# Kernel optimization log

Hardware: AMD Instinct MI355X
Metric: run time of the kernel (lower is better)

The kernel has to match this reference:

```python
import jax, jax.numpy as jnp
import numpy as np

EPS = 1e-5


def setup_inputs() -> dict:
    key = jax.random.key(0)
    ks = jax.random.split(key, 6)
    B, H, W, C = 4, 64, 64, 64
    x_in = jax.random.normal(ks[0], (B, H, W, C), dtype=jnp.float32)
    scale = 1.0 / np.sqrt(C)
    w1 = jax.random.normal(ks[1], (C, C), dtype=jnp.float32) * scale
    w2 = jax.random.normal(ks[2], (C, C), dtype=jnp.float32) * scale
    w3 = jax.random.normal(ks[3], (C, C), dtype=jnp.float32) * scale
    w4 = jax.random.normal(ks[4], (C, C), dtype=jnp.float32) * scale
    zeros = jnp.zeros((C,), dtype=jnp.float32)
    return {
        "x_in": x_in,
        "w1": w1, "w2": w2, "w3": w3, "w4": w4,
        "b1": zeros, "b2": zeros, "b3": zeros, "b4": zeros,
        "gamma": jnp.ones((C,), dtype=jnp.float32),
        "beta": zeros,
    }


def reference(x_in, w1, w2, w3, w4, b1, b2, b3, b4, gamma, beta):
    B, H, W, C = x_in.shape
    # BatchNorm over batch + spatial dims, per channel (training-mode batch stats)
    mean = jnp.mean(x_in, axis=(0, 1, 2))            # [C]
    var = jnp.var(x_in, axis=(0, 1, 2))              # [C]
    x = (x_in - mean) * jax.lax.rsqrt(var + EPS) * gamma + beta
    # QKV projections
    q = jnp.einsum('bhwc,cC->bhwC', x, w1) + b1
    k = jnp.einsum('bhwc,cC->bhwC', x, w2) + b2
    v = jnp.einsum('bhwc,cC->bhwC', x, w3) + b3
    # Full spatial attention: [B, H, W, H, W]
    sdpa = jnp.einsum('bhwc,bHWc->bhwHW', q, k) / jnp.sqrt(jnp.float32(C))
    sdpa = jax.nn.softmax(sdpa.reshape(B, H, W, H * W), axis=-1)
    sdpa = sdpa.reshape(B, H, W, H, W)
    x = jnp.einsum('bhwHW,bHWc->bhwc', sdpa, v)
    # Output projection + residual
    x = jnp.einsum('bhwc,cC->bhwC', x, w4) + b4
    return x + x_in
```

## Files before the change

### kernel.cpp

```cpp
#include <hip/hip_runtime.h>

typedef _Float16 f16;
typedef _Float16 half8 __attribute__((ext_vector_type(8)));
typedef float f32x4 __attribute__((ext_vector_type(4)));
typedef float f32x16 __attribute__((ext_vector_type(16)));
typedef unsigned u32x4 __attribute__((ext_vector_type(4)));

#define LDW 72

__global__ __launch_bounds__(256) void k_bnstats(const float* __restrict__ x, float* __restrict__ part){
    __shared__ float red[512];
    int t = threadIdx.x;
    int c = t & 63, rg = t >> 6;
    int rb = blockIdx.x * 64;
    float s = 0.f, s2 = 0.f;
    for(int r = rg; r < 64; r += 4){
        float v = x[(rb + r) * 64 + c];
        s += v; s2 += v * v;
    }
    red[t] = s; red[256 + t] = s2;
    __syncthreads();
    if(t < 128){
        int c2 = t & 63, h = t >> 6;
        float a = red[h * 256 + c2] + red[h * 256 + c2 + 64] + red[h * 256 + c2 + 128] + red[h * 256 + c2 + 192];
        part[blockIdx.x * 128 + t] = a;
    }
}

__global__ __launch_bounds__(256) void k_qkv(
    const float* __restrict__ x,
    const float* __restrict__ w1, const float* __restrict__ w2, const float* __restrict__ w3,
    const float* __restrict__ b1, const float* __restrict__ b2, const float* __restrict__ b3,
    const float* __restrict__ gamma, const float* __restrict__ beta,
    const float* __restrict__ part,
    f16* __restrict__ Q, f16* __restrict__ Kx, f16* __restrict__ Vt){
    __shared__ f16 wT[3 * 64 * LDW];
    __shared__ float sc[64], sh[64], bb[3][64];
    __shared__ float psum[128];
    int t = threadIdx.x;
    for(int i = t; i < 3 * 4096; i += 256){
        int j = i >> 12, e = i & 4095, k = e >> 6, n = e & 63;
        const float* wp = (j == 0) ? w1 : ((j == 1) ? w2 : w3);
        wT[j * 64 * LDW + n * LDW + k] = (f16)wp[e];
    }
    if(t < 128){
        float a0 = 0.f, a1 = 0.f, a2 = 0.f, a3 = 0.f;
        for(int b = 0; b < 256; b += 4){
            a0 += part[b * 128 + t];       a1 += part[(b + 1) * 128 + t];
            a2 += part[(b + 2) * 128 + t]; a3 += part[(b + 3) * 128 + t];
        }
        psum[t] = (a0 + a1) + (a2 + a3);
    }
    __syncthreads();
    if(t < 64){
        float mean = psum[t] * (1.f / 16384.f);
        float var  = psum[64 + t] * (1.f / 16384.f) - mean * mean;
        float s = gamma[t] * rsqrtf(var + 1e-5f);
        sc[t] = s;
        sh[t] = beta[t] - mean * s;
        bb[0][t] = b1[t]; bb[1][t] = b2[t]; bb[2][t] = b3[t];
    }
    __syncthreads();
    int w = t >> 6, lane = t & 63, quad = lane >> 4, l15 = lane & 15;
    int rowb = blockIdx.x * 64 + w * 16;
    int arow = rowb + l15;
    half8 a[2];
    #pragma unroll
    for(int kc = 0; kc < 2; kc++){
        f32x4 x0 = *(const f32x4*)&x[arow * 64 + kc * 32 + quad * 8];
        f32x4 x1 = *(const f32x4*)&x[arow * 64 + kc * 32 + quad * 8 + 4];
        half8 h;
        #pragma unroll
        for(int j = 0; j < 8; j++){
            int c = kc * 32 + quad * 8 + j;
            float xv = (j < 4) ? x0[j & 3] : x1[j & 3];
            h[j] = (f16)(xv * sc[c] + sh[c]);
        }
        a[kc] = h;
    }
    const f32x4 vzero = {0.f, 0.f, 0.f, 0.f};
    f32x4 acc[3][4];
    #pragma unroll
    for(int m = 0; m < 3; m++){
        #pragma unroll
        for(int nt = 0; nt < 4; nt++){
            acc[m][nt] = vzero;
            #pragma unroll
            for(int kc = 0; kc < 2; kc++){
                half8 bfr = *(half8*)&wT[m * 64 * LDW + (nt * 16 + l15) * LDW + kc * 32 + quad * 8];
                acc[m][nt] = __builtin_amdgcn_mfma_f32_16x16x32_f16(a[kc], bfr, acc[m][nt], 0, 0, 0);
            }
        }
    }
    const float qs = 0.18033688011112043f;
    #pragma unroll
    for(int nt = 0; nt < 4; nt++){
        #pragma unroll
        for(int r = 0; r < 4; r++){
            int row = rowb + quad * 4 + r;
            int col = nt * 16 + l15;
            Q[row * 64 + col]  = (f16)((acc[0][nt][r] + bb[0][col]) * qs);
            Kx[row * 64 + col] = (f16)(acc[1][nt][r] + bb[1][col]);
            Vt[((row >> 12) * 64 + col) * 4096 + (row & 4095)] = (f16)(acc[2][nt][r] + bb[2][col]);
        }
    }
}

__global__ __launch_bounds__(256, 4) void k_attn(
    const f16* __restrict__ Q, const f16* __restrict__ Kx, const f16* __restrict__ Vt,
    f16* __restrict__ Oph, float* __restrict__ lw){
    __shared__ f16 KV[2][2 * 64 * LDW];
    __shared__ float lred[4][32];
    int t = threadIdx.x;
    int kq = blockIdx.x & 7, qg = blockIdx.x >> 3;
    int b = qg >> 5;
    int w = t >> 6, lane = t & 63, l31 = lane & 31, hi = lane >> 5;
    int qrow0 = qg * 128 + w * 32;
    const int BUF = 2 * 64 * LDW;

    half8 aq[4];
    #pragma unroll
    for(int dc = 0; dc < 4; dc++)
        aq[dc] = *(const half8*)&Q[(qrow0 + l31) * 64 + dc * 16 + hi * 8];

    const f16* gsrc[4];
    int loff[4], gstep[4];
    #pragma unroll
    for(int i = 0; i < 4; i++){
        int idx = t + i * 256;
        int rr = (idx >> 3) & 63, c8 = idx & 7, kt0 = kq * 8;
        if(idx < 512){
            loff[i] = rr * LDW + c8 * 8;
            gsrc[i] = &Kx[(b * 4096 + kt0 * 64 + rr) * 64 + c8 * 8];
            gstep[i] = 64 * 64;
        } else {
            loff[i] = 64 * LDW + rr * LDW + c8 * 8;
            gsrc[i] = &Vt[(b * 64 + rr) * 4096 + kt0 * 64 + c8 * 8];
            gstep[i] = 64;
        }
    }
    half8 pre[4];
    #pragma unroll
    for(int i = 0; i < 4; i++){ pre[i] = *(const half8*)gsrc[i]; gsrc[i] += gstep[i]; }
    #pragma unroll
    for(int i = 0; i < 4; i++) *(half8*)&KV[0][loff[i]] = pre[i];

    f32x16 o[2];
    #pragma unroll
    for(int dt = 0; dt < 2; dt++)
        #pragma unroll
        for(int r = 0; r < 16; r++) o[dt][r] = 0.f;
    float lp = 0.f;

    __syncthreads();
    int cur = 0;
    for(int j = 0; j < 8; j++){
        if(j < 7){
            #pragma unroll
            for(int i = 0; i < 4; i++){ pre[i] = *(const half8*)gsrc[i]; gsrc[i] += gstep[i]; }
        }
        const f16* Kb = &KV[0][0] + cur * BUF;
        const f16* Vb = Kb + 64 * LDW;
        #pragma unroll
        for(int kt = 0; kt < 2; kt++){
            half8 ak[4];
            #pragma unroll
            for(int dc = 0; dc < 4; dc++)
                ak[dc] = *(const half8*)&Kb[(kt * 32 + l31) * LDW + dc * 16 + hi * 8];
            half8 vb[2][2];
            #pragma unroll
            for(int kc = 0; kc < 2; kc++)
                #pragma unroll
                for(int dt = 0; dt < 2; dt++)
                    vb[kc][dt] = *(const half8*)&Vb[(dt * 32 + l31) * LDW + kt * 32 + kc * 16 + hi * 8];
            f32x16 s;
            #pragma unroll
            for(int r = 0; r < 16; r++) s[r] = 0.f;
            #pragma unroll
            for(int dc = 0; dc < 4; dc++)
                s = __builtin_amdgcn_mfma_f32_32x32x16_f16(ak[dc], aq[dc], s, 0, 0, 0);
            float pf[16], ls = 0.f;
            #pragma unroll
            for(int r = 0; r < 16; r++){
                float p = __builtin_amdgcn_exp2f(fminf(s[r], 15.f));
                pf[r] = p; ls += p;
            }
            lp += ls;
            unsigned wv[4][2];
            #pragma unroll
            for(int g = 0; g < 4; g++){
                wv[g][0] = __builtin_bit_cast(unsigned, __builtin_amdgcn_cvt_pkrtz(pf[4*g+0], pf[4*g+1]));
                wv[g][1] = __builtin_bit_cast(unsigned, __builtin_amdgcn_cvt_pkrtz(pf[4*g+2], pf[4*g+3]));
            }
            #pragma unroll
            for(int kc = 0; kc < 2; kc++){
                unsigned x0 = wv[2*kc][0], y0 = wv[2*kc+1][0];
                unsigned x1 = wv[2*kc][1], y1 = wv[2*kc+1][1];
                asm("v_permlane32_swap_b32 %0, %1" : "+v"(x0), "+v"(y0));
                asm("v_permlane32_swap_b32 %0, %1" : "+v"(x1), "+v"(y1));
                u32x4 pw = {x0, x1, y0, y1};
                half8 pa = __builtin_bit_cast(half8, pw);
                #pragma unroll
                for(int dt = 0; dt < 2; dt++)
                    o[dt] = __builtin_amdgcn_mfma_f32_32x32x16_f16(pa, vb[kc][dt], o[dt], 0, 0, 0);
            }
        }
        if(j < 7){
            f16* wb = &KV[0][0] + (cur ^ 1) * BUF;
            #pragma unroll
            for(int i = 0; i < 4; i++) *(half8*)(wb + loff[i]) = pre[i];
        }
        cur ^= 1;
        __syncthreads();
    }
    {
        float v = lp + __shfl_xor(lp, 32);
        if(hi == 0){
            int row = qrow0 + l31;
            lw[kq * 16384 + row] = v;
            lred[w][l31] = __builtin_amdgcn_rcpf(v);
        }
    }
    #pragma unroll
    for(int r = 0; r < 16; r++){
        int qrl = (r & 3) + 8 * (r >> 2) + 4 * hi;
        float inv = lred[w][qrl];
        int row = qrow0 + qrl;
        #pragma unroll
        for(int dt = 0; dt < 2; dt++)
            Oph[kq * 1048576 + row * 64 + dt * 32 + l31] = (f16)(o[dt][r] * inv);
    }
}

__global__ __launch_bounds__(256) void k_merge(
    const f16* __restrict__ Oph, const float* __restrict__ lw,
    const float* __restrict__ w4, const float* __restrict__ b4,
    const float* __restrict__ x, float* __restrict__ out){
    __shared__ f16 Om[64 * LDW];
    __shared__ f16 wT[64 * LDW];
    __shared__ float b4f[64];
    int t = threadIdx.x;
    int rb = blockIdx.x * 64;
    for(int i = t; i < 4096; i += 256){
        int k = i >> 6, n = i & 63;
        wT[n * LDW + k] = (f16)w4[i];
    }
    if(t < 64) b4f[t] = b4[t];
    for(int i = t; i < 512; i += 256){
        int row = i >> 3, c8 = i & 7;
        int gr = rb + row;
        float num[8] = {0.f,0.f,0.f,0.f,0.f,0.f,0.f,0.f};
        float den = 0.f;
        #pragma unroll
        for(int s = 0; s < 8; s++){
            float li = lw[s * 16384 + gr];
            half8 ov = *(const half8*)&Oph[s * 1048576 + gr * 64 + c8 * 8];
            #pragma unroll
            for(int j = 0; j < 8; j++) num[j] += li * (float)ov[j];
            den += li;
        }
        float invd = 1.f / den;
        #pragma unroll
        for(int j = 0; j < 8; j++) Om[row * LDW + c8 * 8 + j] = (f16)(num[j] * invd);
    }
    __syncthreads();
    int w = t >> 6, lane = t & 63, quad = lane >> 4, l15 = lane & 15;
    half8 a[2];
    #pragma unroll
    for(int kc = 0; kc < 2; kc++)
        a[kc] = *(half8*)&Om[(w * 16 + l15) * LDW + kc * 32 + quad * 8];
    #pragma unroll
    for(int nt = 0; nt < 4; nt++){
        f32x4 y = {0.f, 0.f, 0.f, 0.f};
        #pragma unroll
        for(int kc = 0; kc < 2; kc++){
            half8 bfr = *(half8*)&wT[(nt * 16 + l15) * LDW + kc * 32 + quad * 8];
            y = __builtin_amdgcn_mfma_f32_16x16x32_f16(a[kc], bfr, y, 0, 0, 0);
        }
        #pragma unroll
        for(int r = 0; r < 4; r++){
            int row = rb + w * 16 + quad * 4 + r;
            int col = nt * 16 + l15;
            out[row * 64 + col] = y[r] + b4f[col] + x[row * 64 + col];
        }
    }
}

extern "C" void kernel_launch(void* const* d_in, const int* in_sizes, int n_in,
                              void* d_out, int out_size, void* d_ws, size_t ws_size,
                              hipStream_t stream){
    (void)in_sizes; (void)n_in; (void)out_size; (void)ws_size;
    const float* x  = (const float*)d_in[0];
    const float* w1 = (const float*)d_in[1];
    const float* w2 = (const float*)d_in[2];
    const float* w3 = (const float*)d_in[3];
    const float* w4 = (const float*)d_in[4];
    const float* b1 = (const float*)d_in[5];
    const float* b2 = (const float*)d_in[6];
    const float* b3 = (const float*)d_in[7];
    const float* b4 = (const float*)d_in[8];
    const float* gm = (const float*)d_in[9];
    const float* bt = (const float*)d_in[10];
    char* ws = (char*)d_ws;
    f16* Q    = (f16*)(ws);
    f16* Kx   = (f16*)(ws + (size_t)(2u << 20));
    f16* Vt   = (f16*)(ws + (size_t)(4u << 20));
    float* part = (float*)(ws + (size_t)(6u << 20));
    f16* Oph  = (f16*)(ws + (size_t)(8u << 20));
    float* lwp = (float*)(ws + (size_t)(24u << 20));

    hipLaunchKernelGGL(k_bnstats, dim3(256),  dim3(256), 0, stream, x, part);
    hipLaunchKernelGGL(k_qkv,     dim3(256),  dim3(256), 0, stream, x, w1, w2, w3, b1, b2, b3, gm, bt, part, Q, Kx, Vt);
    hipLaunchKernelGGL(k_attn,    dim3(1024), dim3(256), 0, stream, Q, Kx, Vt, Oph, lwp);
    hipLaunchKernelGGL(k_merge,   dim3(256),  dim3(256), 0, stream, Oph, lwp, w4, b4, x, (float*)d_out);
}
```

Measured before the change: 130.9 us.

## Fuse BN stats into QKV via grid barrier and merge into attention tail

Removes the separate BN-statistics kernel: each QKV block reduces its own rows, atomically adds into global sums, and spins on a global counter until all 256 blocks have contributed before normalizing. The merge/output-projection kernel is also folded into the attention kernel, where the last of the 8 key-split blocks per query group (tracked by an atomic counter) combines the partial outputs and applies w4, bias and residual. This cuts two kernel launches and their inter-kernel gaps, at the cost of a memset, atomics, a spin-wait that assumes all 256 QKV blocks are co-resident, and a serialized merge tail on the last-arriving blocks.

```diff
diff --git a/kernel.cpp b/kernel.cpp
--- a/kernel.cpp
+++ b/kernel.cpp
@@ -8,49 +8,55 @@
 
 #define LDW 72
 
-__global__ __launch_bounds__(256) void k_bnstats(const float* __restrict__ x, float* __restrict__ part){
-    __shared__ float red[512];
-    int t = threadIdx.x;
-    int c = t & 63, rg = t >> 6;
-    int rb = blockIdx.x * 64;
-    float s = 0.f, s2 = 0.f;
-    for(int r = rg; r < 64; r += 4){
-        float v = x[(rb + r) * 64 + c];
-        s += v; s2 += v * v;
-    }
-    red[t] = s; red[256 + t] = s2;
-    __syncthreads();
-    if(t < 128){
-        int c2 = t & 63, h = t >> 6;
-        float a = red[h * 256 + c2] + red[h * 256 + c2 + 64] + red[h * 256 + c2 + 128] + red[h * 256 + c2 + 192];
-        part[blockIdx.x * 128 + t] = a;
-    }
-}
-
 __global__ __launch_bounds__(256) void k_qkv(
     const float* __restrict__ x,
     const float* __restrict__ w1, const float* __restrict__ w2, const float* __restrict__ w3,
     const float* __restrict__ b1, const float* __restrict__ b2, const float* __restrict__ b3,
     const float* __restrict__ gamma, const float* __restrict__ beta,
-    const float* __restrict__ part,
+    float* __restrict__ sums, unsigned* __restrict__ ctr, unsigned* __restrict__ mergecnt,
     f16* __restrict__ Q, f16* __restrict__ Kx, f16* __restrict__ Vt){
     __shared__ f16 wT[3 * 64 * LDW];
     __shared__ float sc[64], sh[64], bb[3][64];
+    __shared__ float red[512];
     __shared__ float psum[128];
     int t = threadIdx.x;
+    int bid = blockIdx.x;
+
+    {
+        int c = t & 63, rg = t >> 6;
+        int rb = bid * 64;
+        float s = 0.f, s2 = 0.f;
+        for(int r = rg; r < 64; r += 4){
+            float v = x[(rb + r) * 64 + c];
+            s += v; s2 += v * v;
+        }
+        red[t] = s; red[256 + t] = s2;
+    }
+    if(t == 0 && bid < 128) mergecnt[bid] = 0u;
+    __syncthreads();
+    if(t < 128){
+        int c2 = t & 63, h = t >> 6;
+        float a = red[h * 256 + c2] + red[h * 256 + c2 + 64] + red[h * 256 + c2 + 128] + red[h * 256 + c2 + 192];
+        atomicAdd(&sums[t], a);
+    }
+    if(t == 0){
+        __threadfence();
+        atomicAdd(ctr, 1u);
+    }
     for(int i = t; i < 3 * 4096; i += 256){
         int j = i >> 12, e = i & 4095, k = e >> 6, n = e & 63;
         const float* wp = (j == 0) ? w1 : ((j == 1) ? w2 : w3);
         wT[j * 64 * LDW + n * LDW + k] = (f16)wp[e];
     }
-    if(t < 128){
-        float a0 = 0.f, a1 = 0.f, a2 = 0.f, a3 = 0.f;
-        for(int b = 0; b < 256; b += 4){
-            a0 += part[b * 128 + t];       a1 += part[(b + 1) * 128 + t];
-            a2 += part[(b + 2) * 128 + t]; a3 += part[(b + 3) * 128 + t];
-        }
-        psum[t] = (a0 + a1) + (a2 + a3);
-    }
+    if(t < 64){ bb[0][t] = b1[t]; bb[1][t] = b2[t]; bb[2][t] = b3[t]; }
+    if(t == 0){
+        while(__hip_atomic_load(ctr, __ATOMIC_RELAXED, __HIP_MEMORY_SCOPE_AGENT) < 256u){
+            __builtin_amdgcn_s_sleep(8);
+        }
+    }
+    __syncthreads();
+    if(t < 128)
+        psum[t] = __hip_atomic_load(&sums[t], __ATOMIC_RELAXED, __HIP_MEMORY_SCOPE_AGENT);
     __syncthreads();
     if(t < 64){
         float mean = psum[t] * (1.f / 16384.f);
@@ -58,11 +64,11 @@
         float s = gamma[t] * rsqrtf(var + 1e-5f);
         sc[t] = s;
         sh[t] = beta[t] - mean * s;
-        bb[0][t] = b1[t]; bb[1][t] = b2[t]; bb[2][t] = b3[t];
-    }
-    __syncthreads();
+    }
+    __syncthreads();
+
     int w = t >> 6, lane = t & 63, quad = lane >> 4, l15 = lane & 15;
-    int rowb = blockIdx.x * 64 + w * 16;
+    int rowb = bid * 64 + w * 16;
     int arow = rowb + l15;
     half8 a[2];
     #pragma unroll
@@ -108,15 +114,20 @@
 
 __global__ __launch_bounds__(256, 4) void k_attn(
     const f16* __restrict__ Q, const f16* __restrict__ Kx, const f16* __restrict__ Vt,
-    f16* __restrict__ Oph, float* __restrict__ lw){
-    __shared__ f16 KV[2][2 * 64 * LDW];
-    __shared__ float lred[4][32];
+    f16* __restrict__ Oph, float* __restrict__ lw,
+    const float* __restrict__ w4, const float* __restrict__ b4,
+    const float* __restrict__ x, float* __restrict__ out,
+    unsigned* __restrict__ mergecnt){
+    __shared__ char smem[37892] __attribute__((aligned(16)));
+    f16* KVs  = (f16*)smem;
+    float* lred = (float*)(smem + 36864);
+    int* isLastP = (int*)(smem + 37376);
+    const int BUF = 2 * 64 * LDW;
     int t = threadIdx.x;
     int kq = blockIdx.x & 7, qg = blockIdx.x >> 3;
     int b = qg >> 5;
     int w = t >> 6, lane = t & 63, l31 = lane & 31, hi = lane >> 5;
     int qrow0 = qg * 128 + w * 32;
-    const int BUF = 2 * 64 * LDW;
 
     half8 aq[4];
     #pragma unroll
@@ -143,7 +154,7 @@
     #pragma unroll
     for(int i = 0; i < 4; i++){ pre[i] = *(const half8*)gsrc[i]; gsrc[i] += gstep[i]; }
     #pragma unroll
-    for(int i = 0; i < 4; i++) *(half8*)&KV[0][loff[i]] = pre[i];
+    for(int i = 0; i < 4; i++) *(half8*)&KVs[loff[i]] = pre[i];
 
     f32x16 o[2];
     #pragma unroll
@@ -159,7 +170,7 @@
             #pragma unroll
             for(int i = 0; i < 4; i++){ pre[i] = *(const half8*)gsrc[i]; gsrc[i] += gstep[i]; }
         }
-        const f16* Kb = &KV[0][0] + cur * BUF;
+        const f16* Kb = KVs + cur * BUF;
         const f16* Vb = Kb + 64 * LDW;
         #pragma unroll
         for(int kt = 0; kt < 2; kt++){
@@ -206,7 +217,7 @@
             }
         }
         if(j < 7){
-            f16* wb = &KV[0][0] + (cur ^ 1) * BUF;
+            f16* wb = KVs + (cur ^ 1) * BUF;
             #pragma unroll
             for(int i = 0; i < 4; i++) *(half8*)(wb + loff[i]) = pre[i];
         }
@@ -218,35 +229,39 @@
         if(hi == 0){
             int row = qrow0 + l31;
             lw[kq * 16384 + row] = v;
-            lred[w][l31] = __builtin_amdgcn_rcpf(v);
+            lred[w * 32 + l31] = __builtin_amdgcn_rcpf(v);
         }
     }
     #pragma unroll
     for(int r = 0; r < 16; r++){
         int qrl = (r & 3) + 8 * (r >> 2) + 4 * hi;
-        float inv = lred[w][qrl];
+        float inv = lred[w * 32 + qrl];
         int row = qrow0 + qrl;
         #pragma unroll
         for(int dt = 0; dt < 2; dt++)
             Oph[kq * 1048576 + row * 64 + dt * 32 + l31] = (f16)(o[dt][r] * inv);
     }
-}
-
-__global__ __launch_bounds__(256) void k_merge(
-    const f16* __restrict__ Oph, const float* __restrict__ lw,
-    const float* __restrict__ w4, const float* __restrict__ b4,
-    const float* __restrict__ x, float* __restrict__ out){
-    __shared__ f16 Om[64 * LDW];
-    __shared__ f16 wT[64 * LDW];
-    __shared__ float b4f[64];
-    int t = threadIdx.x;
-    int rb = blockIdx.x * 64;
+
+    __threadfence();
+    __syncthreads();
+    if(t == 0){
+        unsigned old = atomicAdd(&mergecnt[qg], 1u);
+        *isLastP = (old == 7u);
+    }
+    __syncthreads();
+    if(!*isLastP) return;
+    __threadfence();
+
+    f16* Om   = (f16*)smem;
+    f16* wT4  = (f16*)(smem + 18432);
+    float* b4f = (float*)(smem + 27648);
+    int rb = qg * 128;
     for(int i = t; i < 4096; i += 256){
         int k = i >> 6, n = i & 63;
-        wT[n * LDW + k] = (f16)w4[i];
+        wT4[n * LDW + k] = (f16)w4[i];
     }
     if(t < 64) b4f[t] = b4[t];
-    for(int i = t; i < 512; i += 256){
+    for(int i = t; i < 1024; i += 256){
         int row = i >> 3, c8 = i & 7;
         int gr = rb + row;
         float num[8] = {0.f,0.f,0.f,0.f,0.f,0.f,0.f,0.f};
@@ -264,24 +279,28 @@
         for(int j = 0; j < 8; j++) Om[row * LDW + c8 * 8 + j] = (f16)(num[j] * invd);
     }
     __syncthreads();
-    int w = t >> 6, lane = t & 63, quad = lane >> 4, l15 = lane & 15;
-    half8 a[2];
-    #pragma unroll
-    for(int kc = 0; kc < 2; kc++)
-        a[kc] = *(half8*)&Om[(w * 16 + l15) * LDW + kc * 32 + quad * 8];
-    #pragma unroll
-    for(int nt = 0; nt < 4; nt++){
-        f32x4 y = {0.f, 0.f, 0.f, 0.f};
-        #pragma unroll
-        for(int kc = 0; kc < 2; kc++){
-            half8 bfr = *(half8*)&wT[(nt * 16 + l15) * LDW + kc * 32 + quad * 8];
-            y = __builtin_amdgcn_mfma_f32_16x16x32_f16(a[kc], bfr, y, 0, 0, 0);
-        }
-        #pragma unroll
-        for(int r = 0; r < 4; r++){
-            int row = rb + w * 16 + quad * 4 + r;
-            int col = nt * 16 + l15;
-            out[row * 64 + col] = y[r] + b4f[col] + x[row * 64 + col];
+    int quad = lane >> 4, l15 = lane & 15;
+    #pragma unroll
+    for(int rt = 0; rt < 2; rt++){
+        int rloc = w * 32 + rt * 16;
+        half8 a[2];
+        #pragma unroll
+        for(int kc = 0; kc < 2; kc++)
+            a[kc] = *(half8*)&Om[(rloc + l15) * LDW + kc * 32 + quad * 8];
+        #pragma unroll
+        for(int nt = 0; nt < 4; nt++){
+            f32x4 y = {0.f, 0.f, 0.f, 0.f};
+            #pragma unroll
+            for(int kc = 0; kc < 2; kc++){
+                half8 bfr = *(half8*)&wT4[(nt * 16 + l15) * LDW + kc * 32 + quad * 8];
+                y = __builtin_amdgcn_mfma_f32_16x16x32_f16(a[kc], bfr, y, 0, 0, 0);
+            }
+            #pragma unroll
+            for(int r = 0; r < 4; r++){
+                int row = rb + rloc + quad * 4 + r;
+                int col = nt * 16 + l15;
+                out[row * 64 + col] = y[r] + b4f[col] + x[row * 64 + col];
+            }
         }
     }
 }
@@ -305,12 +324,15 @@
     f16* Q    = (f16*)(ws);
     f16* Kx   = (f16*)(ws + (size_t)(2u << 20));
     f16* Vt   = (f16*)(ws + (size_t)(4u << 20));
-    float* part = (float*)(ws + (size_t)(6u << 20));
+    float* sums = (float*)(ws + (size_t)(6u << 20));
+    unsigned* ctr = (unsigned*)(ws + (size_t)(6u << 20) + 512);
+    unsigned* mergecnt = (unsigned*)(ws + (size_t)(6u << 20) + 1024);
     f16* Oph  = (f16*)(ws + (size_t)(8u << 20));
     float* lwp = (float*)(ws + (size_t)(24u << 20));
 
-    hipLaunchKernelGGL(k_bnstats, dim3(256),  dim3(256), 0, stream, x, part);
-    hipLaunchKernelGGL(k_qkv,     dim3(256),  dim3(256), 0, stream, x, w1, w2, w3, b1, b2, b3, gm, bt, part, Q, Kx, Vt);
-    hipLaunchKernelGGL(k_attn,    dim3(1024), dim3(256), 0, stream, Q, Kx, Vt, Oph, lwp);
-    hipLaunchKernelGGL(k_merge,   dim3(256),  dim3(256), 0, stream, Oph, lwp, w4, b4, x, (float*)d_out);
+    hipMemsetAsync(ws + (size_t)(6u << 20), 0, 2048, stream);
+    hipLaunchKernelGGL(k_qkv,  dim3(256),  dim3(256), 0, stream,
+                       x, w1, w2, w3, b1, b2, b3, gm, bt, sums, ctr, mergecnt, Q, Kx, Vt);
+    hipLaunchKernelGGL(k_attn, dim3(1024), dim3(256), 0, stream,
+                       Q, Kx, Vt, Oph, lwp, w4, b4, x, (float*)d_out, mergecnt);
 }
```

After: 307.7 us. +135.1%, slower.

## Fuse BN stats into QKV kernel via atomic grid barrier; add MFMA setprio

Applied to the files above, without the earlier changes.

Removes the separate batch-norm statistics kernel. Each QKV block now computes its partial sums, atomically adds them to a global buffer, and spins on a global counter until all 256 blocks have contributed. The kernel launch and the serial reduction over 256 partials go away, replaced by a memset, atomics and a grid-wide spin-wait. The wait assumes all 256 blocks are co-resident. The attention kernel also raises wave priority around its MFMA sections using s_setprio.

```diff
diff --git a/kernel.cpp b/kernel.cpp
--- a/kernel.cpp
+++ b/kernel.cpp
@@ -8,49 +8,54 @@
 
 #define LDW 72
 
-__global__ __launch_bounds__(256) void k_bnstats(const float* __restrict__ x, float* __restrict__ part){
-    __shared__ float red[512];
-    int t = threadIdx.x;
-    int c = t & 63, rg = t >> 6;
-    int rb = blockIdx.x * 64;
-    float s = 0.f, s2 = 0.f;
-    for(int r = rg; r < 64; r += 4){
-        float v = x[(rb + r) * 64 + c];
-        s += v; s2 += v * v;
-    }
-    red[t] = s; red[256 + t] = s2;
-    __syncthreads();
-    if(t < 128){
-        int c2 = t & 63, h = t >> 6;
-        float a = red[h * 256 + c2] + red[h * 256 + c2 + 64] + red[h * 256 + c2 + 128] + red[h * 256 + c2 + 192];
-        part[blockIdx.x * 128 + t] = a;
-    }
-}
-
 __global__ __launch_bounds__(256) void k_qkv(
     const float* __restrict__ x,
     const float* __restrict__ w1, const float* __restrict__ w2, const float* __restrict__ w3,
     const float* __restrict__ b1, const float* __restrict__ b2, const float* __restrict__ b3,
     const float* __restrict__ gamma, const float* __restrict__ beta,
-    const float* __restrict__ part,
+    float* __restrict__ sums, unsigned* __restrict__ ctr,
     f16* __restrict__ Q, f16* __restrict__ Kx, f16* __restrict__ Vt){
     __shared__ f16 wT[3 * 64 * LDW];
     __shared__ float sc[64], sh[64], bb[3][64];
+    __shared__ float red[512];
     __shared__ float psum[128];
     int t = threadIdx.x;
+    int bid = blockIdx.x;
+
+    {
+        int c = t & 63, rg = t >> 6;
+        int rb = bid * 64;
+        float s = 0.f, s2 = 0.f;
+        for(int r = rg; r < 64; r += 4){
+            float v = x[(rb + r) * 64 + c];
+            s += v; s2 += v * v;
+        }
+        red[t] = s; red[256 + t] = s2;
+    }
+    __syncthreads();
+    if(t < 128){
+        int c2 = t & 63, h = t >> 6;
+        float a = red[h * 256 + c2] + red[h * 256 + c2 + 64] + red[h * 256 + c2 + 128] + red[h * 256 + c2 + 192];
+        atomicAdd(&sums[t], a);
+    }
+    __syncthreads();
+    if(t == 0)
+        __hip_atomic_fetch_add(ctr, 1u, __ATOMIC_RELEASE, __HIP_MEMORY_SCOPE_AGENT);
+
     for(int i = t; i < 3 * 4096; i += 256){
         int j = i >> 12, e = i & 4095, k = e >> 6, n = e & 63;
         const float* wp = (j == 0) ? w1 : ((j == 1) ? w2 : w3);
         wT[j * 64 * LDW + n * LDW + k] = (f16)wp[e];
     }
-    if(t < 128){
-        float a0 = 0.f, a1 = 0.f, a2 = 0.f, a3 = 0.f;
-        for(int b = 0; b < 256; b += 4){
-            a0 += part[b * 128 + t];       a1 += part[(b + 1) * 128 + t];
-            a2 += part[(b + 2) * 128 + t]; a3 += part[(b + 3) * 128 + t];
-        }
-        psum[t] = (a0 + a1) + (a2 + a3);
-    }
+    if(t < 64){ bb[0][t] = b1[t]; bb[1][t] = b2[t]; bb[2][t] = b3[t]; }
+
+    if(t == 0){
+        while(__hip_atomic_load(ctr, __ATOMIC_ACQUIRE, __HIP_MEMORY_SCOPE_AGENT) < 256u)
+            __builtin_amdgcn_s_sleep(4);
+    }
+    __syncthreads();
+    if(t < 128)
+        psum[t] = __hip_atomic_load(&sums[t], __ATOMIC_RELAXED, __HIP_MEMORY_SCOPE_AGENT);
     __syncthreads();
     if(t < 64){
         float mean = psum[t] * (1.f / 16384.f);
@@ -58,11 +63,11 @@
         float s = gamma[t] * rsqrtf(var + 1e-5f);
         sc[t] = s;
         sh[t] = beta[t] - mean * s;
-        bb[0][t] = b1[t]; bb[1][t] = b2[t]; bb[2][t] = b3[t];
-    }
-    __syncthreads();
+    }
+    __syncthreads();
+
     int w = t >> 6, lane = t & 63, quad = lane >> 4, l15 = lane & 15;
-    int rowb = blockIdx.x * 64 + w * 16;
+    int rowb = bid * 64 + w * 16;
     int arow = rowb + l15;
     half8 a[2];
     #pragma unroll
@@ -173,12 +178,14 @@
                 #pragma unroll
                 for(int dt = 0; dt < 2; dt++)
                     vb[kc][dt] = *(const half8*)&Vb[(dt * 32 + l31) * LDW + kt * 32 + kc * 16 + hi * 8];
+            __builtin_amdgcn_s_setprio(1);
             f32x16 s;
             #pragma unroll
             for(int r = 0; r < 16; r++) s[r] = 0.f;
             #pragma unroll
             for(int dc = 0; dc < 4; dc++)
                 s = __builtin_amdgcn_mfma_f32_32x32x16_f16(ak[dc], aq[dc], s, 0, 0, 0);
+            __builtin_amdgcn_s_setprio(0);
             float pf[16], ls = 0.f;
             #pragma unroll
             for(int r = 0; r < 16; r++){
@@ -192,6 +199,7 @@
                 wv[g][0] = __builtin_bit_cast(unsigned, __builtin_amdgcn_cvt_pkrtz(pf[4*g+0], pf[4*g+1]));
                 wv[g][1] = __builtin_bit_cast(unsigned, __builtin_amdgcn_cvt_pkrtz(pf[4*g+2], pf[4*g+3]));
             }
+            __builtin_amdgcn_s_setprio(1);
             #pragma unroll
             for(int kc = 0; kc < 2; kc++){
                 unsigned x0 = wv[2*kc][0], y0 = wv[2*kc+1][0];
@@ -204,6 +212,7 @@
                 for(int dt = 0; dt < 2; dt++)
                     o[dt] = __builtin_amdgcn_mfma_f32_32x32x16_f16(pa, vb[kc][dt], o[dt], 0, 0, 0);
             }
+            __builtin_amdgcn_s_setprio(0);
         }
         if(j < 7){
             f16* wb = &KV[0][0] + (cur ^ 1) * BUF;
@@ -305,12 +314,14 @@
     f16* Q    = (f16*)(ws);
     f16* Kx   = (f16*)(ws + (size_t)(2u << 20));
     f16* Vt   = (f16*)(ws + (size_t)(4u << 20));
-    float* part = (float*)(ws + (size_t)(6u << 20));
+    float* sums = (float*)(ws + (size_t)(6u << 20));
+    unsigned* ctr = (unsigned*)(ws + (size_t)(6u << 20) + 512);
     f16* Oph  = (f16*)(ws + (size_t)(8u << 20));
     float* lwp = (float*)(ws + (size_t)(24u << 20));
 
-    hipLaunchKernelGGL(k_bnstats, dim3(256),  dim3(256), 0, stream, x, part);
-    hipLaunchKernelGGL(k_qkv,     dim3(256),  dim3(256), 0, stream, x, w1, w2, w3, b1, b2, b3, gm, bt, part, Q, Kx, Vt);
-    hipLaunchKernelGGL(k_attn,    dim3(1024), dim3(256), 0, stream, Q, Kx, Vt, Oph, lwp);
-    hipLaunchKernelGGL(k_merge,   dim3(256),  dim3(256), 0, stream, Oph, lwp, w4, b4, x, (float*)d_out);
+    hipMemsetAsync(ws + (size_t)(6u << 20), 0, 1024, stream);
+    hipLaunchKernelGGL(k_qkv,  dim3(256),  dim3(256), 0, stream,
+                       x, w1, w2, w3, b1, b2, b3, gm, bt, sums, ctr, Q, Kx, Vt);
+    hipLaunchKernelGGL(k_attn, dim3(1024), dim3(256), 0, stream, Q, Kx, Vt, Oph, lwp);
+    hipLaunchKernelGGL(k_merge, dim3(256), dim3(256), 0, stream, Oph, lwp, w4, b4, x, (float*)d_out);
 }
```

Result: no change. 133.4 us (+1.9%).

## Fuse split-KV merge and output projection into attention kernel via intra-block split

Applied to the files above, without the earlier changes.

The attention kernel now gives each block 32 query rows, and its four waves each process a quarter of the keys with private double-buffered LDS tiles, so the per-iteration block barrier is gone. The partial outputs and row sums are combined in shared memory, and the block then applies the w4 projection, bias and residual directly. This removes the separate merge kernel and the fp16 partial-output round trip through global memory. In exchange the grid drops to 512 blocks with 72KB of LDS each, which lowers occupancy and puts a serial reduction plus projection tail at the end of each block.

```diff
diff --git a/kernel.cpp b/kernel.cpp
--- a/kernel.cpp
+++ b/kernel.cpp
@@ -7,6 +7,7 @@
 typedef unsigned u32x4 __attribute__((ext_vector_type(4)));
 
 #define LDW 72
+#define LDV 36
 
 __global__ __launch_bounds__(256) void k_bnstats(const float* __restrict__ x, float* __restrict__ part){
     __shared__ float red[512];
@@ -106,44 +107,53 @@
     }
 }
 
-__global__ __launch_bounds__(256, 4) void k_attn(
+__global__ __launch_bounds__(256, 2) void k_attn(
     const f16* __restrict__ Q, const f16* __restrict__ Kx, const f16* __restrict__ Vt,
-    f16* __restrict__ Oph, float* __restrict__ lw){
-    __shared__ f16 KV[2][2 * 64 * LDW];
-    __shared__ float lred[4][32];
-    int t = threadIdx.x;
-    int kq = blockIdx.x & 7, qg = blockIdx.x >> 3;
-    int b = qg >> 5;
-    int w = t >> 6, lane = t & 63, l31 = lane & 31, hi = lane >> 5;
-    int qrow0 = qg * 128 + w * 32;
-    const int BUF = 2 * 64 * LDW;
+    const float* __restrict__ w4, const float* __restrict__ b4,
+    const float* __restrict__ x, float* __restrict__ out){
+    __shared__ char smem[73728] __attribute__((aligned(16)));
+    f16* KVf = (f16*)smem;
+    int t = threadIdx.x, bid = blockIdx.x;
+    int w = t >> 6, lane = t & 63, l31 = lane & 31, hi = lane >> 5, quad = lane >> 4, l15 = lane & 15;
+    int b = bid >> 7;
+    int qrow0 = bid * 32;
+    int kvbase = w * 1024;
+    const int WSTR = 9216;
+    const int BSTR = 4608;
+    int wbase = w * WSTR;
+
+    f16 wreg[16];
+    #pragma unroll
+    for(int i = 0; i < 16; i++) wreg[i] = (f16)w4[t + i * 256];
 
     half8 aq[4];
     #pragma unroll
     for(int dc = 0; dc < 4; dc++)
         aq[dc] = *(const half8*)&Q[(qrow0 + l31) * 64 + dc * 16 + hi * 8];
 
-    const f16* gsrc[4];
-    int loff[4], gstep[4];
-    #pragma unroll
-    for(int i = 0; i < 4; i++){
-        int idx = t + i * 256;
-        int rr = (idx >> 3) & 63, c8 = idx & 7, kt0 = kq * 8;
-        if(idx < 512){
-            loff[i] = rr * LDW + c8 * 8;
-            gsrc[i] = &Kx[(b * 4096 + kt0 * 64 + rr) * 64 + c8 * 8];
-            gstep[i] = 64 * 64;
+    const f16* gsrc[8];
+    int loff[8], gstep[8];
+    #pragma unroll
+    for(int i = 0; i < 8; i++){
+        int idx = lane + i * 64;
+        if(idx < 256){
+            int rr = idx >> 3, c8 = idx & 7;
+            loff[i]  = wbase + rr * LDW + c8 * 8;
+            gsrc[i]  = &Kx[(b * 4096 + kvbase + rr) * 64 + c8 * 8];
+            gstep[i] = 32 * 64;
         } else {
-            loff[i] = 64 * LDW + rr * LDW + c8 * 8;
-            gsrc[i] = &Vt[(b * 64 + rr) * 4096 + kt0 * 64 + c8 * 8];
-            gstep[i] = 64;
-        }
-    }
-    half8 pre[4];
-    #pragma unroll
-    for(int i = 0; i < 4; i++){ pre[i] = *(const half8*)gsrc[i]; gsrc[i] += gstep[i]; }
-    #pragma unroll
-    for(int i = 0; i < 4; i++) *(half8*)&KV[0][loff[i]] = pre[i];
+            int v = idx - 256;
+            int rr = v >> 2, c4 = v & 3;
+            loff[i]  = wbase + 32 * LDW + rr * LDV + c4 * 8;
+            gsrc[i]  = &Vt[(b * 64 + rr) * 4096 + kvbase + c4 * 8];
+            gstep[i] = 32;
+        }
+    }
+    half8 pre[8];
+    #pragma unroll
+    for(int i = 0; i < 8; i++){ pre[i] = *(const half8*)gsrc[i]; gsrc[i] += gstep[i]; }
+    #pragma unroll
+    for(int i = 0; i < 8; i++) *(half8*)&KVf[loff[i]] = pre[i];
 
     f32x16 o[2];
     #pragma unroll
@@ -152,136 +162,122 @@
         for(int r = 0; r < 16; r++) o[dt][r] = 0.f;
     float lp = 0.f;
 
-    __syncthreads();
     int cur = 0;
-    for(int j = 0; j < 8; j++){
-        if(j < 7){
-            #pragma unroll
-            for(int i = 0; i < 4; i++){ pre[i] = *(const half8*)gsrc[i]; gsrc[i] += gstep[i]; }
-        }
-        const f16* Kb = &KV[0][0] + cur * BUF;
-        const f16* Vb = Kb + 64 * LDW;
-        #pragma unroll
-        for(int kt = 0; kt < 2; kt++){
-            half8 ak[4];
-            #pragma unroll
-            for(int dc = 0; dc < 4; dc++)
-                ak[dc] = *(const half8*)&Kb[(kt * 32 + l31) * LDW + dc * 16 + hi * 8];
-            half8 vb[2][2];
-            #pragma unroll
-            for(int kc = 0; kc < 2; kc++)
+    for(int j = 0; j < 32; j++){
+        if(j < 31){
+            #pragma unroll
+            for(int i = 0; i < 8; i++){ pre[i] = *(const half8*)gsrc[i]; gsrc[i] += gstep[i]; }
+        }
+        const f16* Kb = KVf + wbase + cur * BSTR;
+        const f16* Vb = Kb + 32 * LDW;
+        half8 ak[4];
+        #pragma unroll
+        for(int dc = 0; dc < 4; dc++)
+            ak[dc] = *(const half8*)&Kb[l31 * LDW + dc * 16 + hi * 8];
+        half8 vb[2][2];
+        #pragma unroll
+        for(int kc = 0; kc < 2; kc++)
+            #pragma unroll
+            for(int dt = 0; dt < 2; dt++)
+                vb[kc][dt] = *(const half8*)&Vb[(dt * 32 + l31) * LDV + kc * 16 + hi * 8];
+        f32x16 s;
+        #pragma unroll
+        for(int r = 0; r < 16; r++) s[r] = 0.f;
+        #pragma unroll
+        for(int dc = 0; dc < 4; dc++)
+            s = __builtin_amdgcn_mfma_f32_32x32x16_f16(ak[dc], aq[dc], s, 0, 0, 0);
+        float pf[16], ls = 0.f;
+        #pragma unroll
+        for(int r = 0; r < 16; r++){
+            float p = __builtin_amdgcn_exp2f(fminf(s[r], 15.f));
+            pf[r] = p; ls += p;
+        }
+        lp += ls;
+        unsigned wv[4][2];
+        #pragma unroll
+        for(int g = 0; g < 4; g++){
+            wv[g][0] = __builtin_bit_cast(unsigned, __builtin_amdgcn_cvt_pkrtz(pf[4*g+0], pf[4*g+1]));
+            wv[g][1] = __builtin_bit_cast(unsigned, __builtin_amdgcn_cvt_pkrtz(pf[4*g+2], pf[4*g+3]));
+        }
+        #pragma unroll
+        for(int kc = 0; kc < 2; kc++){
+            unsigned x0 = wv[2*kc][0], y0 = wv[2*kc+1][0];
+            unsigned x1 = wv[2*kc][1], y1 = wv[2*kc+1][1];
+            asm("v_permlane32_swap_b32 %0, %1" : "+v"(x0), "+v"(y0));
+            asm("v_permlane32_swap_b32 %0, %1" : "+v"(x1), "+v"(y1));
+            u32x4 pw = {x0, x1, y0, y1};
+            half8 pa = __builtin_bit_cast(half8, pw);
+            #pragma unroll
+            for(int dt = 0; dt < 2; dt++)
+                o[dt] = __builtin_amdgcn_mfma_f32_32x32x16_f16(pa, vb[kc][dt], o[dt], 0, 0, 0);
+        }
+        if(j < 31){
+            f16* wb = KVf + (cur ^ 1) * BSTR;
+            #pragma unroll
+            for(int i = 0; i < 8; i++) *(half8*)(wb + loff[i]) = pre[i];
+        }
+        cur ^= 1;
+    }
+
+    float v = lp + __shfl_xor(lp, 32);
+    if(w > 0){
+        float* op  = (float*)(smem + w * 18432);
+        float* lpp = (float*)(smem + w * 18432 + 8192);
+        #pragma unroll
+        for(int r = 0; r < 16; r++){
+            int qrl = (r & 3) + 8 * (r >> 2) + 4 * hi;
+            #pragma unroll
+            for(int dt = 0; dt < 2; dt++)
+                op[qrl * 64 + dt * 32 + l31] = o[dt][r];
+        }
+        if(hi == 0) lpp[l31] = v;
+    }
+    __syncthreads();
+    f16* wT4 = (f16*)smem;
+    #pragma unroll
+    for(int i = 0; i < 16; i++){
+        int idx = t + i * 256, k = idx >> 6, n = idx & 63;
+        wT4[n * LDW + k] = wreg[i];
+    }
+    f16* Om = (f16*)(smem + 9216);
+    if(w == 0){
+        float vtot = v;
+        #pragma unroll
+        for(int m = 1; m < 4; m++) vtot += ((const float*)(smem + m * 18432 + 8192))[l31];
+        #pragma unroll
+        for(int r = 0; r < 16; r++){
+            int qrl = (r & 3) + 8 * (r >> 2) + 4 * hi;
+            float inv = __builtin_amdgcn_rcpf(__shfl(vtot, qrl));
+            #pragma unroll
+            for(int dt = 0; dt < 2; dt++){
+                float tot = o[dt][r];
                 #pragma unroll
-                for(int dt = 0; dt < 2; dt++)
-                    vb[kc][dt] = *(const half8*)&Vb[(dt * 32 + l31) * LDW + kt * 32 + kc * 16 + hi * 8];
-            f32x16 s;
-            #pragma unroll
-            for(int r = 0; r < 16; r++) s[r] = 0.f;
-            #pragma unroll
-            for(int dc = 0; dc < 4; dc++)
-                s = __builtin_amdgcn_mfma_f32_32x32x16_f16(ak[dc], aq[dc], s, 0, 0, 0);
-            float pf[16], ls = 0.f;
-            #pragma unroll
-            for(int r = 0; r < 16; r++){
-                float p = __builtin_amdgcn_exp2f(fminf(s[r], 15.f));
-                pf[r] = p; ls += p;
+                for(int m = 1; m < 4; m++)
+                    tot += ((const float*)(smem + m * 18432))[qrl * 64 + dt * 32 + l31];
+                Om[qrl * LDW + dt * 32 + l31] = (f16)(tot * inv);
             }
-            lp += ls;
-            unsigned wv[4][2];
-            #pragma unroll
-            for(int g = 0; g < 4; g++){
-                wv[g][0] = __builtin_bit_cast(unsigned, __builtin_amdgcn_cvt_pkrtz(pf[4*g+0], pf[4*g+1]));
-                wv[g][1] = __builtin_bit_cast(unsigned, __builtin_amdgcn_cvt_pkrtz(pf[4*g+2], pf[4*g+3]));
+        }
+    }
+    __syncthreads();
+    if(w < 2){
+        half8 a[2];
+        #pragma unroll
+        for(int kc = 0; kc < 2; kc++)
+            a[kc] = *(half8*)&Om[(w * 16 + l15) * LDW + kc * 32 + quad * 8];
+        #pragma unroll
+        for(int nt = 0; nt < 4; nt++){
+            f32x4 y = {0.f, 0.f, 0.f, 0.f};
+            #pragma unroll
+            for(int kc = 0; kc < 2; kc++){
+                half8 bfr = *(half8*)&wT4[(nt * 16 + l15) * LDW + kc * 32 + quad * 8];
+                y = __builtin_amdgcn_mfma_f32_16x16x32_f16(a[kc], bfr, y, 0, 0, 0);
             }
             #pragma unroll
-            for(int kc = 0; kc < 2; kc++){
-                unsigned x0 = wv[2*kc][0], y0 = wv[2*kc+1][0];
-                unsigned x1 = wv[2*kc][1], y1 = wv[2*kc+1][1];
-                asm("v_permlane32_swap_b32 %0, %1" : "+v"(x0), "+v"(y0));
-                asm("v_permlane32_swap_b32 %0, %1" : "+v"(x1), "+v"(y1));
-                u32x4 pw = {x0, x1, y0, y1};
-                half8 pa = __builtin_bit_cast(half8, pw);
-                #pragma unroll
-                for(int dt = 0; dt < 2; dt++)
-                    o[dt] = __builtin_amdgcn_mfma_f32_32x32x16_f16(pa, vb[kc][dt], o[dt], 0, 0, 0);
+            for(int r = 0; r < 4; r++){
+                int row = qrow0 + w * 16 + quad * 4 + r;
+                int col = nt * 16 + l15;
+                out[row * 64 + col] = y[r] + b4[col] + x[row * 64 + col];
             }
-        }
-        if(j < 7){
-            f16* wb = &KV[0][0] + (cur ^ 1) * BUF;
-            #pragma unroll
-            for(int i = 0; i < 4; i++) *(half8*)(wb + loff[i]) = pre[i];
-        }
-        cur ^= 1;
-        __syncthreads();
-    }
-    {
-        float v = lp + __shfl_xor(lp, 32);
-        if(hi == 0){
-            int row = qrow0 + l31;
-            lw[kq * 16384 + row] = v;
-            lred[w][l31] = __builtin_amdgcn_rcpf(v);
-        }
-    }
-    #pragma unroll
-    for(int r = 0; r < 16; r++){
-        int qrl = (r & 3) + 8 * (r >> 2) + 4 * hi;
-        float inv = lred[w][qrl];
-        int row = qrow0 + qrl;
-        #pragma unroll
-        for(int dt = 0; dt < 2; dt++)
-            Oph[kq * 1048576 + row * 64 + dt * 32 + l31] = (f16)(o[dt][r] * inv);
-    }
-}
-
-__global__ __launch_bounds__(256) void k_merge(
-    const f16* __restrict__ Oph, const float* __restrict__ lw,
-    const float* __restrict__ w4, const float* __restrict__ b4,
-    const float* __restrict__ x, float* __restrict__ out){
-    __shared__ f16 Om[64 * LDW];
-    __shared__ f16 wT[64 * LDW];
-    __shared__ float b4f[64];
-    int t = threadIdx.x;
-    int rb = blockIdx.x * 64;
-    for(int i = t; i < 4096; i += 256){
-        int k = i >> 6, n = i & 63;
-        wT[n * LDW + k] = (f16)w4[i];
-    }
-    if(t < 64) b4f[t] = b4[t];
-    for(int i = t; i < 512; i += 256){
-        int row = i >> 3, c8 = i & 7;
-        int gr = rb + row;
-        float num[8] = {0.f,0.f,0.f,0.f,0.f,0.f,0.f,0.f};
-        float den = 0.f;
-        #pragma unroll
-        for(int s = 0; s < 8; s++){
-            float li = lw[s * 16384 + gr];
-            half8 ov = *(const half8*)&Oph[s * 1048576 + gr * 64 + c8 * 8];
-            #pragma unroll
-            for(int j = 0; j < 8; j++) num[j] += li * (float)ov[j];
-            den += li;
-        }
-        float invd = 1.f / den;
-        #pragma unroll
-        for(int j = 0; j < 8; j++) Om[row * LDW + c8 * 8 + j] = (f16)(num[j] * invd);
-    }
-    __syncthreads();
-    int w = t >> 6, lane = t & 63, quad = lane >> 4, l15 = lane & 15;
-    half8 a[2];
-    #pragma unroll
-    for(int kc = 0; kc < 2; kc++)
-        a[kc] = *(half8*)&Om[(w * 16 + l15) * LDW + kc * 32 + quad * 8];
-    #pragma unroll
-    for(int nt = 0; nt < 4; nt++){
-        f32x4 y = {0.f, 0.f, 0.f, 0.f};
-        #pragma unroll
-        for(int kc = 0; kc < 2; kc++){
-            half8 bfr = *(half8*)&wT[(nt * 16 + l15) * LDW + kc * 32 + quad * 8];
-            y = __builtin_amdgcn_mfma_f32_16x16x32_f16(a[kc], bfr, y, 0, 0, 0);
-        }
-        #pragma unroll
-        for(int r = 0; r < 4; r++){
-            int row = rb + w * 16 + quad * 4 + r;
-            int col = nt * 16 + l15;
-            out[row * 64 + col] = y[r] + b4f[col] + x[row * 64 + col];
         }
     }
 }
@@ -306,11 +302,8 @@
     f16* Kx   = (f16*)(ws + (size_t)(2u << 20));
     f16* Vt   = (f16*)(ws + (size_t)(4u << 20));
     float* part = (float*)(ws + (size_t)(6u << 20));
-    f16* Oph  = (f16*)(ws + (size_t)(8u << 20));
-    float* lwp = (float*)(ws + (size_t)(24u << 20));
-
-    hipLaunchKernelGGL(k_bnstats, dim3(256),  dim3(256), 0, stream, x, part);
-    hipLaunchKernelGGL(k_qkv,     dim3(256),  dim3(256), 0, stream, x, w1, w2, w3, b1, b2, b3, gm, bt, part, Q, Kx, Vt);
-    hipLaunchKernelGGL(k_attn,    dim3(1024), dim3(256), 0, stream, Q, Kx, Vt, Oph, lwp);
-    hipLaunchKernelGGL(k_merge,   dim3(256),  dim3(256), 0, stream, Oph, lwp, w4, b4, x, (float*)d_out);
+
+    hipLaunchKernelGGL(k_bnstats, dim3(256), dim3(256), 0, stream, x, part);
+    hipLaunchKernelGGL(k_qkv,     dim3(256), dim3(256), 0, stream, x, w1, w2, w3, b1, b2, b3, gm, bt, part, Q, Kx, Vt);
+    hipLaunchKernelGGL(k_attn,    dim3(512), dim3(256), 0, stream, Q, Kx, Vt, w4, b4, x, (float*)d_out);
 }
```

Measured after the change: 160.8 us. 22.9% more time.
